# Kernel optimization log

Measured on AMD Instinct MI355X. Metric: run time of the kernel, lower is better.

Reference implementation:

```python
import jax, jax.numpy as jnp
import numpy as np

N = 50000
HEADS = 3
NEG_SLOPE = 0.2


def _add_self_loops(edge_index, num_nodes):
    loops = jnp.arange(num_nodes, dtype=edge_index.dtype)
    return jnp.concatenate([edge_index, jnp.stack([loops, loops])], axis=1)


def _gcn_conv(x, edge_index, W, b):
    # PyG GCNConv: add self loops, symmetric deg^-1/2 normalization.
    ei = _add_self_loops(edge_index, x.shape[0])
    src, dst = ei[0], ei[1]
    deg = jax.ops.segment_sum(jnp.ones_like(dst, dtype=x.dtype), dst, num_segments=x.shape[0])
    dinv = jax.lax.rsqrt(deg)  # deg >= 1 due to self loops
    norm = dinv[src] * dinv[dst]                      # [E']
    xw = x @ W                                        # [N, F_out]
    out = jax.ops.segment_sum(xw[src] * norm[:, None], dst, num_segments=x.shape[0])
    return out + b


def _gat_conv(x, edge_index, W, att_src, att_dst, b):
    # PyG GATConv (concat=True): self loops, per-edge attention, segment softmax.
    n = x.shape[0]
    ei = _add_self_loops(edge_index, n)
    src, dst = ei[0], ei[1]
    h = (x @ W).reshape(n, HEADS, -1)                 # [N, H, C]
    a_s = (h * att_src).sum(-1)                       # [N, H]
    a_d = (h * att_dst).sum(-1)                       # [N, H]
    e = jax.nn.leaky_relu(a_s[src] + a_d[dst], NEG_SLOPE)   # [E', H]
    m = jax.ops.segment_max(e, dst, num_segments=n)   # [N, H] per-dst max
    e = jnp.exp(e - m[dst])
    s = jax.ops.segment_sum(e, dst, num_segments=n)   # [N, H]
    alpha = e / s[dst]                                # [E', H]
    out = jax.ops.segment_sum(h[src] * alpha[:, :, None], dst, num_segments=n)
    return out.reshape(n, -1) + b                     # [N, H*C]


def setup_inputs() -> dict:
    key = jax.random.key(0)
    ks = jax.random.split(key, 9)
    in_ch, out_ch = 256, 64
    hid = 2 * out_ch  # 128
    E = 800000
    x = jax.random.normal(ks[0], (N, in_ch), dtype=jnp.float32)
    edge_index = jax.random.randint(ks[1], (2, E), 0, N, dtype=jnp.int32)
    W1 = jax.random.normal(ks[2], (in_ch, hid), dtype=jnp.float32) / np.sqrt(in_ch)
    b1 = jnp.zeros((hid,), dtype=jnp.float32)
    W2 = jax.random.normal(ks[3], (hid, HEADS * out_ch), dtype=jnp.float32) / np.sqrt(hid)
    att_src = jax.random.normal(ks[4], (HEADS, out_ch), dtype=jnp.float32) / np.sqrt(out_ch)
    att_dst = jax.random.normal(ks[5], (HEADS, out_ch), dtype=jnp.float32) / np.sqrt(out_ch)
    b2 = jnp.zeros((HEADS * out_ch,), dtype=jnp.float32)
    return {"x": x, "edge_index": edge_index, "W1": W1, "b1": b1,
            "W2": W2, "att_src": att_src, "att_dst": att_dst, "b2": b2}


def reference(x, edge_index, W1, b1, W2, att_src, att_dst, b2):
    h = jax.nn.relu(_gcn_conv(x, edge_index, W1, b1))
    # F.dropout(training=False) is identity in eval mode
    h = _gat_conv(h, edge_index, W2, att_src, att_dst, b2)
    return jax.nn.relu(h)
```

## Files before the change

kernel.cpp:

```cpp
#include <hip/hip_runtime.h>
#include <hip/hip_fp16.h>
#include <math.h>

#define NODES    50000
#define IN_CH    256
#define HID      128
#define HEADS    3
#define HC       64
#define OC       (HEADS*HC)
#define OCP      256
#define NEG_SLOPE 0.2f

typedef _Float16 half8_t __attribute__((ext_vector_type(8)));
typedef _Float16 half4_t __attribute__((ext_vector_type(4)));
typedef float float4_t __attribute__((ext_vector_type(4)));

__device__ __forceinline__ float lrelu(float v) { return v > 0.f ? v : NEG_SLOPE * v; }

__device__ __forceinline__ unsigned fkey(float f) {
    unsigned b = __float_as_uint(f);
    return (b & 0x80000000u) ? ~b : (b | 0x80000000u);
}
__device__ __forceinline__ float fdec(unsigned k) {
    unsigned b = (k & 0x80000000u) ? (k ^ 0x80000000u) : ~k;
    return __uint_as_float(b);
}


__global__ __launch_bounds__(256) void k_hist(const int* __restrict__ dst, int E, int* __restrict__ cnt,
                                              const float* __restrict__ W1, const float* __restrict__ W2,
                                              _Float16* __restrict__ W1t, _Float16* __restrict__ W2t) {
    int e = blockIdx.x * 256 + threadIdx.x;
    if (e < E) atomicAdd(&cnt[dst[e]], 1);
    if (e < IN_CH * HID) {
        int c = e >> 8, k = e & 255;
        W1t[e] = (_Float16)W1[(size_t)k * HID + c];
    } else if (e < IN_CH * HID + HID * OC) {
        int u = e - IN_CH * HID;
        int c = u >> 7, k = u & 127;
        W2t[u] = (_Float16)W2[(size_t)k * OC + c];
    }
}

__global__ __launch_bounds__(1024) void k_scanA(const int* __restrict__ cnt, int* __restrict__ off,
                                                float* __restrict__ dinv, int* __restrict__ bsum, int n) {
    __shared__ int wsums[16];
    int tid = threadIdx.x, lane = tid & 63, wid = tid >> 6;
    int i = blockIdx.x * 1024 + tid;
    int v = (i < n) ? cnt[i] : 0;
    int incl = v;
    #pragma unroll
    for (int d = 1; d < 64; d <<= 1) {
        int t = __shfl_up(incl, d, 64);
        if (lane >= d) incl += t;
    }
    if (lane == 63) wsums[wid] = incl;
    __syncthreads();
    if (tid == 0) {
        int run = 0;
        #pragma unroll
        for (int j = 0; j < 16; j++) { int t = wsums[j]; wsums[j] = run; run += t; }
        bsum[blockIdx.x] = run;
    }
    __syncthreads();
    if (i < n) {
        off[i] = wsums[wid] + incl - v;
        dinv[i] = rsqrtf((float)(v + 1));
    }
}

__global__ __launch_bounds__(64) void k_scanB(const int* __restrict__ bsum, int* __restrict__ bbase,
                                              int* __restrict__ off, int nb, int n) {
    int tid = threadIdx.x;
    int v = (tid < nb) ? bsum[tid] : 0;
    int incl = v;
    #pragma unroll
    for (int d = 1; d < 64; d <<= 1) {
        int t = __shfl_up(incl, d, 64);
        if (tid >= d) incl += t;
    }
    bbase[tid] = incl - v;
    if (tid == 63) off[n] = incl;
}

__global__ __launch_bounds__(256) void k_scanC(int* __restrict__ off, const int* __restrict__ bbase, int n) {
    int i = blockIdx.x * 256 + threadIdx.x;
    if (i < n) off[i] += bbase[i >> 10];
}

__global__ __launch_bounds__(256) void k_fill(const int* __restrict__ src, const int* __restrict__ dst, int E,
                                              const int* __restrict__ off, int* __restrict__ fill,
                                              int* __restrict__ csr) {
    int e = blockIdx.x * 256 + threadIdx.x;
    if (e < E) {
        int d = dst[e];
        int p = off[d] + atomicAdd(&fill[d], 1);
        csr[p] = src[e];
    }
}

__global__ __launch_bounds__(256) void k_gemm1m(const float* __restrict__ x, const _Float16* __restrict__ W1t,
                                                const float* __restrict__ dinv,
                                                _Float16* __restrict__ xwh, int n) {
    int wid = threadIdx.x >> 6, lane = threadIdx.x & 63;
    int lrow = lane & 15, kgrp = lane >> 4;
    int arow = blockIdx.x * 64 + wid * 16 + lrow;
    bool rv = arow < n;
    const float* xp = x + (size_t)arow * IN_CH + kgrp * 8;

    float4_t acc[8];
    #pragma unroll
    for (int s = 0; s < 8; s++) acc[s] = (float4_t)(0.f);

    #pragma unroll
    for (int kc = 0; kc < IN_CH; kc += 32) {
        float4 a0, a1;
        if (rv) { a0 = *(const float4*)(xp + kc); a1 = *(const float4*)(xp + kc + 4); }
        else { a0 = make_float4(0.f,0.f,0.f,0.f); a1 = a0; }
        half8_t af;
        af[0]=(_Float16)a0.x; af[1]=(_Float16)a0.y; af[2]=(_Float16)a0.z; af[3]=(_Float16)a0.w;
        af[4]=(_Float16)a1.x; af[5]=(_Float16)a1.y; af[6]=(_Float16)a1.z; af[7]=(_Float16)a1.w;
        #pragma unroll
        for (int s = 0; s < 8; s++) {
            const _Float16* bp = W1t + (size_t)(s * 16 + lrow) * IN_CH + kc + kgrp * 8;
            half8_t bf = *(const half8_t*)bp;
            acc[s] = __builtin_amdgcn_mfma_f32_16x16x32_f16(af, bf, acc[s], 0, 0, 0);
        }
    }

    int orow0 = blockIdx.x * 64 + wid * 16 + kgrp * 4;
    #pragma unroll
    for (int r = 0; r < 4; r++) {
        int orow = orow0 + r;
        if (orow < n) {
            float sc = dinv[orow];
            _Float16* po = xwh + ((size_t)orow << 7) + lrow;
            #pragma unroll
            for (int s = 0; s < 8; s++) po[s * 16] = (_Float16)(sc * acc[s][r]);
        }
    }
}

__global__ __launch_bounds__(256) void k_gcn(const _Float16* __restrict__ xwh, const int* __restrict__ csr,
                                             const int* __restrict__ off, const float* __restrict__ dinv,
                                             const float* __restrict__ b1, _Float16* __restrict__ hh, int n) {
    int w = (blockIdx.x * 256 + threadIdx.x) >> 6;
    int lane = threadIdx.x & 63;
    if (w >= n) return;
    int egrp = lane >> 4;
    int c8 = (lane & 15) * 8;
    float acc[8];
    #pragma unroll
    for (int j = 0; j < 8; j++) acc[j] = 0.f;

    int beg = off[w], end = off[w + 1];
    int i = beg;
    for (; i + 16 <= end; i += 16) {
        int s0 = csr[i + egrp];
        int s1 = csr[i + 4 + egrp];
        int s2 = csr[i + 8 + egrp];
        int s3 = csr[i + 12 + egrp];
        half8_t v0 = *(const half8_t*)(xwh + ((size_t)s0 << 7) + c8);
        half8_t v1 = *(const half8_t*)(xwh + ((size_t)s1 << 7) + c8);
        half8_t v2 = *(const half8_t*)(xwh + ((size_t)s2 << 7) + c8);
        half8_t v3 = *(const half8_t*)(xwh + ((size_t)s3 << 7) + c8);
        half8_t p01 = v0 + v1;
        half8_t p23 = v2 + v3;
        #pragma unroll
        for (int j = 0; j < 8; j++)
            acc[j] += (float)p01[j] + (float)p23[j];
    }
    for (; i + 4 <= end; i += 4) {
        int s = csr[i + egrp];
        half8_t v = *(const half8_t*)(xwh + ((size_t)s << 7) + c8);
        #pragma unroll
        for (int j = 0; j < 8; j++) acc[j] += (float)v[j];
    }
    if (i < end && egrp < (end - i)) {
        int s = csr[i + egrp];
        half8_t v = *(const half8_t*)(xwh + ((size_t)s << 7) + c8);
        #pragma unroll
        for (int j = 0; j < 8; j++) acc[j] += (float)v[j];
    }

    #pragma unroll
    for (int j = 0; j < 8; j++) {
        acc[j] += __shfl_xor(acc[j], 16, 64);
        acc[j] += __shfl_xor(acc[j], 32, 64);
    }
    if (egrp == 0) {
        float di = dinv[w];
        half8_t self = *(const half8_t*)(xwh + ((size_t)w << 7) + c8);
        float4 bb0 = *(const float4*)(b1 + c8);
        float4 bb1 = *(const float4*)(b1 + c8 + 4);
        float bv[8] = {bb0.x, bb0.y, bb0.z, bb0.w, bb1.x, bb1.y, bb1.z, bb1.w};
        half8_t o;
        #pragma unroll
        for (int j = 0; j < 8; j++)
            o[j] = (_Float16)fmaxf(fmaf(di, acc[j] + (float)self[j], bv[j]), 0.f);
        *(half8_t*)(hh + ((size_t)w << 7) + c8) = o;
    }
}

__global__ __launch_bounds__(256) void k_gemm2m(const _Float16* __restrict__ hh, const _Float16* __restrict__ W2t,
                                                _Float16* __restrict__ h2h, int n) {
    int wid = threadIdx.x >> 6, lane = threadIdx.x & 63;
    int lrow = lane & 15, kgrp = lane >> 4;
    int arow = blockIdx.x * 64 + wid * 16 + lrow;
    bool rv = arow < n;
    const _Float16* hp = hh + ((size_t)arow << 7) + kgrp * 8;

    float4_t acc[12];
    #pragma unroll
    for (int s = 0; s < 12; s++) acc[s] = (float4_t)(0.f);

    #pragma unroll
    for (int kc = 0; kc < HID; kc += 32) {
        half8_t af = (half8_t)((_Float16)0.f);
        if (rv) af = *(const half8_t*)(hp + kc);
        #pragma unroll
        for (int s = 0; s < 12; s++) {
            const _Float16* bp = W2t + (size_t)(s * 16 + lrow) * HID + kc + kgrp * 8;
            half8_t bf = *(const half8_t*)bp;
            acc[s] = __builtin_amdgcn_mfma_f32_16x16x32_f16(af, bf, acc[s], 0, 0, 0);
        }
    }

    int orow0 = blockIdx.x * 64 + wid * 16 + kgrp * 4;
    #pragma unroll
    for (int r = 0; r < 4; r++) {
        int orow = orow0 + r;
        if (orow < n) {
            _Float16* po = h2h + ((size_t)orow << 8) + lrow;
            #pragma unroll
            for (int s = 0; s < 12; s++) po[s * 16] = (_Float16)acc[s][r];
        }
    }
}

__global__ __launch_bounds__(256) void k_att(const _Float16* __restrict__ h2h, const float* __restrict__ att_s,
                                             const float* __restrict__ att_d, float* __restrict__ a_s4,
                                             float* __restrict__ a_d4, int n) {
    int w = (blockIdx.x * 256 + threadIdx.x) >> 6;
    int lane = threadIdx.x & 63;
    if (w >= n) return;
    bool act = lane < 48;
    int ll = act ? lane : (lane - 48);
    int hd = ll >> 4;
    int c4 = ll * 4;

    half4_t hv = *(const half4_t*)(h2h + ((size_t)w << 8) + c4);
    float4 as = *(const float4*)(att_s + c4);
    float4 ad = *(const float4*)(att_d + c4);
    float vs = (float)hv[0] * as.x + (float)hv[1] * as.y + (float)hv[2] * as.z + (float)hv[3] * as.w;
    float vd = (float)hv[0] * ad.x + (float)hv[1] * ad.y + (float)hv[2] * ad.z + (float)hv[3] * ad.w;
    #pragma unroll
    for (int o = 1; o < 16; o <<= 1) {
        vs += __shfl_xor(vs, o, 64);
        vd += __shfl_xor(vd, o, 64);
    }
    if (act && (ll & 15) == 0) {
        a_s4[w * 4 + hd] = vs;
        a_d4[w * 4 + hd] = vd;
    }
}

__global__ __launch_bounds__(1024) void k_asmax(const float* __restrict__ a_s4, int n, unsigned* __restrict__ asmaxk) {
    int i = blockIdx.x * 1024 + threadIdx.x;
    float m0 = -1e30f, m1 = -1e30f, m2 = -1e30f;
    if (i < n) {
        float4 v = *(const float4*)(a_s4 + (size_t)i * 4);
        m0 = v.x; m1 = v.y; m2 = v.z;
    }
    #pragma unroll
    for (int o = 32; o > 0; o >>= 1) {
        m0 = fmaxf(m0, __shfl_xor(m0, o, 64));
        m1 = fmaxf(m1, __shfl_xor(m1, o, 64));
        m2 = fmaxf(m2, __shfl_xor(m2, o, 64));
    }
    __shared__ float sm[16][3];
    int lane = threadIdx.x & 63, wid = threadIdx.x >> 6;
    if (lane == 0) { sm[wid][0] = m0; sm[wid][1] = m1; sm[wid][2] = m2; }
    __syncthreads();
    if (threadIdx.x == 0) {
        for (int j = 1; j < 16; j++) {
            m0 = fmaxf(m0, sm[j][0]); m1 = fmaxf(m1, sm[j][1]); m2 = fmaxf(m2, sm[j][2]);
        }
        atomicMax(asmaxk + 0, fkey(m0));
        atomicMax(asmaxk + 1, fkey(m1));
        atomicMax(asmaxk + 2, fkey(m2));
    }
}

#define GAT_EDGE(ev, hv) do { \
    float wl = __expf(lrelu((ev) + adh) - Ch); \
    ssum += wl; \
    a0 = fmaf(wl, (float)(hv)[0], a0); \
    a1 = fmaf(wl, (float)(hv)[1], a1); \
    a2 = fmaf(wl, (float)(hv)[2], a2); \
    a3 = fmaf(wl, (float)(hv)[3], a3); \
} while (0)

__global__ __launch_bounds__(256) void k_gat(const _Float16* __restrict__ h2h, const int* __restrict__ csr,
                                             const int* __restrict__ off, const float* __restrict__ a_s4,
                                             const float* __restrict__ a_d4, const unsigned* __restrict__ asmaxk,
                                             const float* __restrict__ b2, float* __restrict__ out, int n) {
    int w = (blockIdx.x * 256 + threadIdx.x) >> 6;
    int lane = threadIdx.x & 63;
    if (w >= n) return;
    bool act = lane < 48;
    int ll = act ? lane : (lane - 48);
    int hd = ll >> 4;
    int c4 = ll * 4;

    float adh = a_d4[w * 4 + hd];
    float Ch  = lrelu(fdec(asmaxk[hd]) + adh);
    float ash = a_s4[w * 4 + hd];
    float wsl = __expf(lrelu(ash + adh) - Ch);
    float ssum = wsl;
    half4_t hv = *(const half4_t*)(h2h + ((size_t)w << 8) + c4);
    float a0 = wsl * (float)hv[0], a1 = wsl * (float)hv[1];
    float a2 = wsl * (float)hv[2], a3 = wsl * (float)hv[3];

    int beg = off[w], end = off[w + 1];
    int i = beg;
    for (; i + 4 <= end; i += 4) {
        int sA = csr[i], sB = csr[i + 1], sC = csr[i + 2], sD = csr[i + 3];
        float eA = a_s4[(size_t)sA * 4 + hd];
        float eB = a_s4[(size_t)sB * 4 + hd];
        float eC = a_s4[(size_t)sC * 4 + hd];
        float eD = a_s4[(size_t)sD * 4 + hd];
        half4_t hA = *(const half4_t*)(h2h + ((size_t)sA << 8) + c4);
        half4_t hB = *(const half4_t*)(h2h + ((size_t)sB << 8) + c4);
        half4_t hC = *(const half4_t*)(h2h + ((size_t)sC << 8) + c4);
        half4_t hD = *(const half4_t*)(h2h + ((size_t)sD << 8) + c4);
        GAT_EDGE(eA, hA); GAT_EDGE(eB, hB); GAT_EDGE(eC, hC); GAT_EDGE(eD, hD);
    }
    for (; i < end; i++) {
        int s = csr[i];
        float ev = a_s4[(size_t)s * 4 + hd];
        half4_t hx = *(const half4_t*)(h2h + ((size_t)s << 8) + c4);
        GAT_EDGE(ev, hx);
    }

    if (act) {
        float inv = 1.f / ssum;
        float4 bb = *(const float4*)(b2 + c4);
        float4 o;
        o.x = fmaxf(fmaf(a0, inv, bb.x), 0.f);
        o.y = fmaxf(fmaf(a1, inv, bb.y), 0.f);
        o.z = fmaxf(fmaf(a2, inv, bb.z), 0.f);
        o.w = fmaxf(fmaf(a3, inv, bb.w), 0.f);
        *(float4*)(out + (size_t)w * OC + c4) = o;
    }
}

extern "C" void kernel_launch(void* const* d_in, const int* in_sizes, int n_in,
                              void* d_out, int out_size, void* d_ws, size_t ws_size,
                              hipStream_t stream) {
    const float* x        = (const float*)d_in[0];
    const int*   ei       = (const int*)d_in[1];
    const float* W1       = (const float*)d_in[2];
    const float* b1       = (const float*)d_in[3];
    const float* W2       = (const float*)d_in[4];
    const float* att_src  = (const float*)d_in[5];
    const float* att_dst  = (const float*)d_in[6];
    const float* b2       = (const float*)d_in[7];
    float* out = (float*)d_out;

    const int n = in_sizes[0] / IN_CH;
    const int E = in_sizes[1] / 2;
    const int* src = ei;
    const int* dst = ei + E;

    char* ws = (char*)d_ws;
    int*      cnt    = (int*)(ws + 0);
    int*      fill   = (int*)(ws + 200704);
    unsigned* asmaxk = (unsigned*)(ws + 401408);
    int*      off    = (int*)(ws + 401664);
    float*    dinv   = (float*)(ws + 602368);
    int*      bsum   = (int*)(ws + 803072);
    int*      bbase  = (int*)(ws + 803328);
    _Float16* W1t    = (_Float16*)(ws + 803584);
    _Float16* W2t    = (_Float16*)(ws + 869120);
    int*      csr    = (int*)(ws + 918528);
    float*    a_s4   = (float*)(ws + 4118528);
    float*    a_d4   = (float*)(ws + 4918528);
    _Float16* xwh    = (_Float16*)(ws + 5718528);
    _Float16* hh     = (_Float16*)(ws + 18518528);
    _Float16* h2h    = (_Float16*)(ws + 31318528);

    (void)hipMemsetAsync(ws, 0, 401424, stream);

    int egrid = (E + 255) / 256;
    int nb = (n + 1023) / 1024;
    k_hist<<<egrid, 256, 0, stream>>>(dst, E, cnt, W1, W2, W1t, W2t);
    k_scanA<<<nb, 1024, 0, stream>>>(cnt, off, dinv, bsum, n);
    k_scanB<<<1, 64, 0, stream>>>(bsum, bbase, off, nb, n);
    k_scanC<<<(n + 255) / 256, 256, 0, stream>>>(off, bbase, n);
    k_fill<<<egrid, 256, 0, stream>>>(src, dst, E, off, fill, csr);

    int gm = (n + 63) / 64;
    k_gemm1m<<<gm, 256, 0, stream>>>(x, W1t, dinv, xwh, n);

    int ngrid = (n + 3) / 4;
    k_gcn<<<ngrid, 256, 0, stream>>>(xwh, csr, off, dinv, b1, hh, n);

    k_gemm2m<<<gm, 256, 0, stream>>>(hh, W2t, h2h, n);

    k_att<<<ngrid, 256, 0, stream>>>(h2h, att_src, att_dst, a_s4, a_d4, n);
    k_asmax<<<nb, 1024, 0, stream>>>(a_s4, n, asmaxk);
    k_gat<<<ngrid, 256, 0, stream>>>(h2h, csr, off, a_s4, a_d4, asmaxk, b2, out, n);
}
```

Measured before the change: 259.5 us.

## Drop scanC and fill array; use off as atomic cursor and prescale CSR

Removes the k_scanC launch and the separate fill counter array. k_fill now uses atomicAdd on the block-local exclusive offsets plus the per-block base, so after filling, off[w] holds the segment end and segment bounds are rebuilt from off[w-1], off[w] and bbase. CSR entries are stored pre-shifted as byte offsets into h2h, so the gather kernels save the index multiply. The memset also shrinks. This saves one kernel launch and some memory traffic, at the cost of extra bbase lookups and index arithmetic in the gather kernels.

```diff
diff --git a/kernel.cpp b/kernel.cpp
--- a/kernel.cpp
+++ b/kernel.cpp
@@ -70,7 +70,7 @@
 }
 
 __global__ __launch_bounds__(64) void k_scanB(const int* __restrict__ bsum, int* __restrict__ bbase,
-                                              int* __restrict__ off, int nb, int n) {
+                                              int nb) {
     int tid = threadIdx.x;
     int v = (tid < nb) ? bsum[tid] : 0;
     int incl = v;
@@ -80,23 +80,24 @@
         if (tid >= d) incl += t;
     }
     bbase[tid] = incl - v;
-    if (tid == 63) off[n] = incl;
-}
-
-__global__ __launch_bounds__(256) void k_scanC(int* __restrict__ off, const int* __restrict__ bbase, int n) {
-    int i = blockIdx.x * 256 + threadIdx.x;
-    if (i < n) off[i] += bbase[i >> 10];
 }
 
 __global__ __launch_bounds__(256) void k_fill(const int* __restrict__ src, const int* __restrict__ dst, int E,
-                                              const int* __restrict__ off, int* __restrict__ fill,
+                                              int* __restrict__ off, const int* __restrict__ bbase,
                                               int* __restrict__ csr) {
     int e = blockIdx.x * 256 + threadIdx.x;
     if (e < E) {
         int d = dst[e];
-        int p = off[d] + atomicAdd(&fill[d], 1);
-        csr[p] = src[e];
-    }
+        int p = atomicAdd(&off[d], 1) + bbase[d >> 10];
+        csr[p] = src[e] << 9;
+    }
+}
+
+__device__ __forceinline__ int2 seg_of(const int* __restrict__ off, const int* __restrict__ bbase, int w) {
+    int bb = bbase[w >> 10];
+    int beg = ((w & 1023) ? off[w - 1] : 0) + bb;
+    int end = off[w] + bb;
+    return make_int2(beg, end);
 }
 
 __global__ __launch_bounds__(256) void k_gemm1m(const float* __restrict__ x, const _Float16* __restrict__ W1t,
@@ -142,28 +143,31 @@
 }
 
 __global__ __launch_bounds__(256) void k_gcn(const _Float16* __restrict__ xwh, const int* __restrict__ csr,
-                                             const int* __restrict__ off, const float* __restrict__ dinv,
+                                             const int* __restrict__ off, const int* __restrict__ bbase,
+                                             const float* __restrict__ dinv,
                                              const float* __restrict__ b1, _Float16* __restrict__ hh, int n) {
     int w = (blockIdx.x * 256 + threadIdx.x) >> 6;
     int lane = threadIdx.x & 63;
     if (w >= n) return;
     int egrp = lane >> 4;
-    int c8 = (lane & 15) * 8;
+    int c8b = (lane & 15) * 16;
+    const char* xb = (const char*)xwh;
     float acc[8];
     #pragma unroll
     for (int j = 0; j < 8; j++) acc[j] = 0.f;
 
-    int beg = off[w], end = off[w + 1];
+    int2 seg = seg_of(off, bbase, w);
+    int beg = seg.x, end = seg.y;
     int i = beg;
     for (; i + 16 <= end; i += 16) {
-        int s0 = csr[i + egrp];
-        int s1 = csr[i + 4 + egrp];
-        int s2 = csr[i + 8 + egrp];
-        int s3 = csr[i + 12 + egrp];
-        half8_t v0 = *(const half8_t*)(xwh + ((size_t)s0 << 7) + c8);
-        half8_t v1 = *(const half8_t*)(xwh + ((size_t)s1 << 7) + c8);
-        half8_t v2 = *(const half8_t*)(xwh + ((size_t)s2 << 7) + c8);
-        half8_t v3 = *(const half8_t*)(xwh + ((size_t)s3 << 7) + c8);
+        int o0 = csr[i + egrp];
+        int o1 = csr[i + 4 + egrp];
+        int o2 = csr[i + 8 + egrp];
+        int o3 = csr[i + 12 + egrp];
+        half8_t v0 = *(const half8_t*)(xb + (o0 >> 1) + c8b);
+        half8_t v1 = *(const half8_t*)(xb + (o1 >> 1) + c8b);
+        half8_t v2 = *(const half8_t*)(xb + (o2 >> 1) + c8b);
+        half8_t v3 = *(const half8_t*)(xb + (o3 >> 1) + c8b);
         half8_t p01 = v0 + v1;
         half8_t p23 = v2 + v3;
         #pragma unroll
@@ -171,14 +175,14 @@
             acc[j] += (float)p01[j] + (float)p23[j];
     }
     for (; i + 4 <= end; i += 4) {
-        int s = csr[i + egrp];
-        half8_t v = *(const half8_t*)(xwh + ((size_t)s << 7) + c8);
+        int o = csr[i + egrp];
+        half8_t v = *(const half8_t*)(xb + (o >> 1) + c8b);
         #pragma unroll
         for (int j = 0; j < 8; j++) acc[j] += (float)v[j];
     }
     if (i < end && egrp < (end - i)) {
-        int s = csr[i + egrp];
-        half8_t v = *(const half8_t*)(xwh + ((size_t)s << 7) + c8);
+        int o = csr[i + egrp];
+        half8_t v = *(const half8_t*)(xb + (o >> 1) + c8b);
         #pragma unroll
         for (int j = 0; j < 8; j++) acc[j] += (float)v[j];
     }
@@ -190,15 +194,13 @@
     }
     if (egrp == 0) {
         float di = dinv[w];
-        half8_t self = *(const half8_t*)(xwh + ((size_t)w << 7) + c8);
-        float4 bb0 = *(const float4*)(b1 + c8);
-        float4 bb1 = *(const float4*)(b1 + c8 + 4);
-        float bv[8] = {bb0.x, bb0.y, bb0.z, bb0.w, bb1.x, bb1.y, bb1.z, bb1.w};
+        half8_t self = *(const half8_t*)(xb + ((size_t)w << 8) + c8b);
+        const float* bp = (const float*)((const char*)b1 + c8b * 2);
         half8_t o;
         #pragma unroll
         for (int j = 0; j < 8; j++)
-            o[j] = (_Float16)fmaxf(fmaf(di, acc[j] + (float)self[j], bv[j]), 0.f);
-        *(half8_t*)(hh + ((size_t)w << 7) + c8) = o;
+            o[j] = (_Float16)fmaxf(fmaf(di, acc[j] + (float)self[j], bp[j]), 0.f);
+        *(half8_t*)((char*)hh + ((size_t)w << 8) + c8b) = o;
     }
 }
 
@@ -302,7 +304,8 @@
 } while (0)
 
 __global__ __launch_bounds__(256) void k_gat(const _Float16* __restrict__ h2h, const int* __restrict__ csr,
-                                             const int* __restrict__ off, const float* __restrict__ a_s4,
+                                             const int* __restrict__ off, const int* __restrict__ bbase,
+                                             const float* __restrict__ a_s4,
                                              const float* __restrict__ a_d4, const unsigned* __restrict__ asmaxk,
                                              const float* __restrict__ b2, float* __restrict__ out, int n) {
     int w = (blockIdx.x * 256 + threadIdx.x) >> 6;
@@ -311,47 +314,51 @@
     bool act = lane < 48;
     int ll = act ? lane : (lane - 48);
     int hd = ll >> 4;
-    int c4 = ll * 4;
+    int c4b = ll * 8;
+    const char* hb = (const char*)h2h;
+    const char* ab = (const char*)a_s4;
+    int hd4 = hd * 4;
 
     float adh = a_d4[w * 4 + hd];
     float Ch  = lrelu(fdec(asmaxk[hd]) + adh);
     float ash = a_s4[w * 4 + hd];
     float wsl = __expf(lrelu(ash + adh) - Ch);
     float ssum = wsl;
-    half4_t hv = *(const half4_t*)(h2h + ((size_t)w << 8) + c4);
+    half4_t hv = *(const half4_t*)(hb + ((size_t)w << 9) + c4b);
     float a0 = wsl * (float)hv[0], a1 = wsl * (float)hv[1];
     float a2 = wsl * (float)hv[2], a3 = wsl * (float)hv[3];
 
-    int beg = off[w], end = off[w + 1];
+    int2 seg = seg_of(off, bbase, w);
+    int beg = seg.x, end = seg.y;
     int i = beg;
     for (; i + 4 <= end; i += 4) {
-        int sA = csr[i], sB = csr[i + 1], sC = csr[i + 2], sD = csr[i + 3];
-        float eA = a_s4[(size_t)sA * 4 + hd];
-        float eB = a_s4[(size_t)sB * 4 + hd];
-        float eC = a_s4[(size_t)sC * 4 + hd];
-        float eD = a_s4[(size_t)sD * 4 + hd];
-        half4_t hA = *(const half4_t*)(h2h + ((size_t)sA << 8) + c4);
-        half4_t hB = *(const half4_t*)(h2h + ((size_t)sB << 8) + c4);
-        half4_t hC = *(const half4_t*)(h2h + ((size_t)sC << 8) + c4);
-        half4_t hD = *(const half4_t*)(h2h + ((size_t)sD << 8) + c4);
+        int oA = csr[i], oB = csr[i + 1], oC = csr[i + 2], oD = csr[i + 3];
+        float eA = *(const float*)(ab + (oA >> 5) + hd4);
+        float eB = *(const float*)(ab + (oB >> 5) + hd4);
+        float eC = *(const float*)(ab + (oC >> 5) + hd4);
+        float eD = *(const float*)(ab + (oD >> 5) + hd4);
+        half4_t hA = *(const half4_t*)(hb + oA + c4b);
+        half4_t hB = *(const half4_t*)(hb + oB + c4b);
+        half4_t hC = *(const half4_t*)(hb + oC + c4b);
+        half4_t hD = *(const half4_t*)(hb + oD + c4b);
         GAT_EDGE(eA, hA); GAT_EDGE(eB, hB); GAT_EDGE(eC, hC); GAT_EDGE(eD, hD);
     }
     for (; i < end; i++) {
-        int s = csr[i];
-        float ev = a_s4[(size_t)s * 4 + hd];
-        half4_t hx = *(const half4_t*)(h2h + ((size_t)s << 8) + c4);
+        int o = csr[i];
+        float ev = *(const float*)(ab + (o >> 5) + hd4);
+        half4_t hx = *(const half4_t*)(hb + o + c4b);
         GAT_EDGE(ev, hx);
     }
 
     if (act) {
         float inv = 1.f / ssum;
-        float4 bb = *(const float4*)(b2 + c4);
+        const float* bp = (const float*)((const char*)b2 + c4b);
         float4 o;
-        o.x = fmaxf(fmaf(a0, inv, bb.x), 0.f);
-        o.y = fmaxf(fmaf(a1, inv, bb.y), 0.f);
-        o.z = fmaxf(fmaf(a2, inv, bb.z), 0.f);
-        o.w = fmaxf(fmaf(a3, inv, bb.w), 0.f);
-        *(float4*)(out + (size_t)w * OC + c4) = o;
+        o.x = fmaxf(fmaf(a0, inv, bp[0]), 0.f);
+        o.y = fmaxf(fmaf(a1, inv, bp[1]), 0.f);
+        o.z = fmaxf(fmaf(a2, inv, bp[2]), 0.f);
+        o.w = fmaxf(fmaf(a3, inv, bp[3]), 0.f);
+        *(float4*)((char*)out + (size_t)w * (OC * 4) + c4b * 2) = o;
     }
 }
 
@@ -375,40 +382,38 @@
 
     char* ws = (char*)d_ws;
     int*      cnt    = (int*)(ws + 0);
-    int*      fill   = (int*)(ws + 200704);
-    unsigned* asmaxk = (unsigned*)(ws + 401408);
-    int*      off    = (int*)(ws + 401664);
-    float*    dinv   = (float*)(ws + 602368);
-    int*      bsum   = (int*)(ws + 803072);
-    int*      bbase  = (int*)(ws + 803328);
-    _Float16* W1t    = (_Float16*)(ws + 803584);
-    _Float16* W2t    = (_Float16*)(ws + 869120);
-    int*      csr    = (int*)(ws + 918528);
-    float*    a_s4   = (float*)(ws + 4118528);
-    float*    a_d4   = (float*)(ws + 4918528);
-    _Float16* xwh    = (_Float16*)(ws + 5718528);
-    _Float16* hh     = (_Float16*)(ws + 18518528);
-    _Float16* h2h    = (_Float16*)(ws + 31318528);
-
-    (void)hipMemsetAsync(ws, 0, 401424, stream);
+    unsigned* asmaxk = (unsigned*)(ws + 200704);
+    int*      off    = (int*)(ws + 200960);
+    float*    dinv   = (float*)(ws + 401664);
+    int*      bsum   = (int*)(ws + 602368);
+    int*      bbase  = (int*)(ws + 602624);
+    _Float16* W1t    = (_Float16*)(ws + 602880);
+    _Float16* W2t    = (_Float16*)(ws + 668416);
+    int*      csr    = (int*)(ws + 717568);
+    float*    a_s4   = (float*)(ws + 3917568);
+    float*    a_d4   = (float*)(ws + 4717568);
+    _Float16* xwh    = (_Float16*)(ws + 5517568);
+    _Float16* hh     = (_Float16*)(ws + 18317568);
+    _Float16* h2h    = (_Float16*)(ws + 31117568);
+
+    (void)hipMemsetAsync(ws, 0, 200720, stream);
 
     int egrid = (E + 255) / 256;
     int nb = (n + 1023) / 1024;
     k_hist<<<egrid, 256, 0, stream>>>(dst, E, cnt, W1, W2, W1t, W2t);
     k_scanA<<<nb, 1024, 0, stream>>>(cnt, off, dinv, bsum, n);
-    k_scanB<<<1, 64, 0, stream>>>(bsum, bbase, off, nb, n);
-    k_scanC<<<(n + 255) / 256, 256, 0, stream>>>(off, bbase, n);
-    k_fill<<<egrid, 256, 0, stream>>>(src, dst, E, off, fill, csr);
+    k_scanB<<<1, 64, 0, stream>>>(bsum, bbase, nb);
+    k_fill<<<egrid, 256, 0, stream>>>(src, dst, E, off, bbase, csr);
 
     int gm = (n + 63) / 64;
     k_gemm1m<<<gm, 256, 0, stream>>>(x, W1t, dinv, xwh, n);
 
     int ngrid = (n + 3) / 4;
-    k_gcn<<<ngrid, 256, 0, stream>>>(xwh, csr, off, dinv, b1, hh, n);
+    k_gcn<<<ngrid, 256, 0, stream>>>(xwh, csr, off, bbase, dinv, b1, hh, n);
 
     k_gemm2m<<<gm, 256, 0, stream>>>(hh, W2t, h2h, n);
 
     k_att<<<ngrid, 256, 0, stream>>>(h2h, att_src, att_dst, a_s4, a_d4, n);
     k_asmax<<<nb, 1024, 0, stream>>>(a_s4, n, asmaxk);
-    k_gat<<<ngrid, 256, 0, stream>>>(h2h, csr, off, a_s4, a_d4, asmaxk, b2, out, n);
-}
+    k_gat<<<ngrid, 256, 0, stream>>>(h2h, csr, off, bbase, a_s4, a_d4, asmaxk, b2, out, n);
+}
```

Result: slower. 272.2 us (+4.9%).

## Build CSR via two-level bucket sort instead of histogram-scan-fill

Applied to the files above, without the earlier changes.

Replaces the per-node histogram, three-kernel scan and global atomic fill with a coarse bucketing pass (128 destinations per bucket), a single-block bucket scan, and a per-bucket LDS counting sort that writes offsets, dinv and CSR. Global atomics now hit only 391 bucket counters, and most scatter work moves into shared memory, with fewer launches and a smaller memset. The cost is heavy contention on those few bucket counters, a fixed per-bucket capacity of 4096 edges that silently drops overflow on skewed graphs, and 16-bit packing of the source index, which cannot hold node ids of 65536 or more.

```diff
diff --git a/kernel.cpp b/kernel.cpp
--- a/kernel.cpp
+++ b/kernel.cpp
@@ -8,8 +8,9 @@
 #define HEADS    3
 #define HC       64
 #define OC       (HEADS*HC)
-#define OCP      256
 #define NEG_SLOPE 0.2f
+#define NBK      391
+#define BCAP     4096
 
 typedef _Float16 half8_t __attribute__((ext_vector_type(8)));
 typedef _Float16 half4_t __attribute__((ext_vector_type(4)));
@@ -26,12 +27,18 @@
     return __uint_as_float(b);
 }
 
-
-__global__ __launch_bounds__(256) void k_hist(const int* __restrict__ dst, int E, int* __restrict__ cnt,
-                                              const float* __restrict__ W1, const float* __restrict__ W2,
-                                              _Float16* __restrict__ W1t, _Float16* __restrict__ W2t) {
+__global__ __launch_bounds__(256) void k_bucket(const int* __restrict__ src, const int* __restrict__ dst, int E,
+                                                int* __restrict__ bcnt, unsigned* __restrict__ bstage,
+                                                const float* __restrict__ W1, const float* __restrict__ W2,
+                                                _Float16* __restrict__ W1t, _Float16* __restrict__ W2t) {
     int e = blockIdx.x * 256 + threadIdx.x;
-    if (e < E) atomicAdd(&cnt[dst[e]], 1);
+    if (e < E) {
+        int d = dst[e], s = src[e];
+        int b = d >> 7;
+        int pos = atomicAdd(&bcnt[b], 1);
+        if (pos < BCAP)
+            bstage[(size_t)b * BCAP + pos] = ((unsigned)(d & 127) << 16) | (unsigned)s;
+    }
     if (e < IN_CH * HID) {
         int c = e >> 8, k = e & 255;
         W1t[e] = (_Float16)W1[(size_t)k * HID + c];
@@ -42,12 +49,11 @@
     }
 }
 
-__global__ __launch_bounds__(1024) void k_scanA(const int* __restrict__ cnt, int* __restrict__ off,
-                                                float* __restrict__ dinv, int* __restrict__ bsum, int n) {
-    __shared__ int wsums[16];
+__global__ __launch_bounds__(512) void k_bscan(const int* __restrict__ bcnt, int* __restrict__ bbase,
+                                               int* __restrict__ off, int nbk, int n) {
+    __shared__ int wsums[8];
     int tid = threadIdx.x, lane = tid & 63, wid = tid >> 6;
-    int i = blockIdx.x * 1024 + tid;
-    int v = (i < n) ? cnt[i] : 0;
+    int v = (tid < nbk) ? bcnt[tid] : 0;
     int incl = v;
     #pragma unroll
     for (int d = 1; d < 64; d <<= 1) {
@@ -59,43 +65,59 @@
     if (tid == 0) {
         int run = 0;
         #pragma unroll
-        for (int j = 0; j < 16; j++) { int t = wsums[j]; wsums[j] = run; run += t; }
-        bsum[blockIdx.x] = run;
-    }
-    __syncthreads();
-    if (i < n) {
-        off[i] = wsums[wid] + incl - v;
-        dinv[i] = rsqrtf((float)(v + 1));
-    }
-}
-
-__global__ __launch_bounds__(64) void k_scanB(const int* __restrict__ bsum, int* __restrict__ bbase,
-                                              int* __restrict__ off, int nb, int n) {
-    int tid = threadIdx.x;
-    int v = (tid < nb) ? bsum[tid] : 0;
-    int incl = v;
-    #pragma unroll
-    for (int d = 1; d < 64; d <<= 1) {
-        int t = __shfl_up(incl, d, 64);
-        if (tid >= d) incl += t;
-    }
-    bbase[tid] = incl - v;
-    if (tid == 63) off[n] = incl;
-}
-
-__global__ __launch_bounds__(256) void k_scanC(int* __restrict__ off, const int* __restrict__ bbase, int n) {
-    int i = blockIdx.x * 256 + threadIdx.x;
-    if (i < n) off[i] += bbase[i >> 10];
-}
-
-__global__ __launch_bounds__(256) void k_fill(const int* __restrict__ src, const int* __restrict__ dst, int E,
-                                              const int* __restrict__ off, int* __restrict__ fill,
-                                              int* __restrict__ csr) {
-    int e = blockIdx.x * 256 + threadIdx.x;
-    if (e < E) {
-        int d = dst[e];
-        int p = off[d] + atomicAdd(&fill[d], 1);
-        csr[p] = src[e];
+        for (int j = 0; j < 8; j++) { int t = wsums[j]; wsums[j] = run; run += t; }
+    }
+    __syncthreads();
+    int excl = wsums[wid] + incl - v;
+    if (tid < nbk) bbase[tid] = excl;
+    if (tid == nbk - 1) off[n] = excl + v;
+}
+
+__global__ __launch_bounds__(256) void k_bsort(const unsigned* __restrict__ bstage, const int* __restrict__ bcnt,
+                                               const int* __restrict__ bbase, int* __restrict__ off,
+                                               float* __restrict__ dinv, int* __restrict__ csr, int n) {
+    __shared__ int cnt128[128], exc128[128], rank128[128];
+    __shared__ int wtot;
+    int b = blockIdx.x, tid = threadIdx.x;
+    if (tid < 128) { cnt128[tid] = 0; rank128[tid] = 0; }
+    __syncthreads();
+
+    int cntE = bcnt[b];
+    if (cntE > BCAP) cntE = BCAP;
+    const unsigned* st = bstage + (size_t)b * BCAP;
+    for (int i = tid; i < cntE; i += 256)
+        atomicAdd(&cnt128[st[i] >> 16], 1);
+    __syncthreads();
+
+    int v = 0, incl = 0;
+    if (tid < 128) {
+        v = cnt128[tid];
+        incl = v;
+        #pragma unroll
+        for (int d = 1; d < 64; d <<= 1) {
+            int t = __shfl_up(incl, d, 64);
+            if ((tid & 63) >= d) incl += t;
+        }
+        if (tid == 63) wtot = incl;
+    }
+    __syncthreads();
+    int base = bbase[b];
+    if (tid < 128) {
+        int excl = incl - v + (tid >= 64 ? wtot : 0);
+        exc128[tid] = excl;
+        int gd = b * 128 + tid;
+        if (gd < n) {
+            off[gd] = base + excl;
+            dinv[gd] = rsqrtf((float)(v + 1));
+        }
+    }
+    __syncthreads();
+
+    for (int i = tid; i < cntE; i += 256) {
+        unsigned vv = st[i];
+        int ld = vv >> 16, s = vv & 0xffff;
+        int r = atomicAdd(&rank128[ld], 1);
+        csr[base + exc128[ld] + r] = s;
     }
 }
 
@@ -374,31 +396,28 @@
     const int* dst = ei + E;
 
     char* ws = (char*)d_ws;
-    int*      cnt    = (int*)(ws + 0);
-    int*      fill   = (int*)(ws + 200704);
-    unsigned* asmaxk = (unsigned*)(ws + 401408);
-    int*      off    = (int*)(ws + 401664);
-    float*    dinv   = (float*)(ws + 602368);
-    int*      bsum   = (int*)(ws + 803072);
-    int*      bbase  = (int*)(ws + 803328);
-    _Float16* W1t    = (_Float16*)(ws + 803584);
-    _Float16* W2t    = (_Float16*)(ws + 869120);
-    int*      csr    = (int*)(ws + 918528);
-    float*    a_s4   = (float*)(ws + 4118528);
-    float*    a_d4   = (float*)(ws + 4918528);
-    _Float16* xwh    = (_Float16*)(ws + 5718528);
-    _Float16* hh     = (_Float16*)(ws + 18518528);
-    _Float16* h2h    = (_Float16*)(ws + 31318528);
-
-    (void)hipMemsetAsync(ws, 0, 401424, stream);
+    int*      bcnt   = (int*)(ws + 0);
+    unsigned* asmaxk = (unsigned*)(ws + 2048);
+    int*      off    = (int*)(ws + 4096);
+    float*    dinv   = (float*)(ws + 204800);
+    int*      bbase  = (int*)(ws + 405504);
+    _Float16* W1t    = (_Float16*)(ws + 407552);
+    _Float16* W2t    = (_Float16*)(ws + 473088);
+    unsigned* bstage = (unsigned*)(ws + 522240);
+    int*      csr    = (int*)(ws + 6928384);
+    float*    a_s4   = (float*)(ws + 10128384);
+    float*    a_d4   = (float*)(ws + 10928384);
+    _Float16* xwh    = (_Float16*)(ws + 11728384);
+    _Float16* hh     = (_Float16*)(ws + 24528384);
+    _Float16* h2h    = (_Float16*)(ws + 37328384);
+
+    (void)hipMemsetAsync(ws, 0, 2064, stream);
 
     int egrid = (E + 255) / 256;
     int nb = (n + 1023) / 1024;
-    k_hist<<<egrid, 256, 0, stream>>>(dst, E, cnt, W1, W2, W1t, W2t);
-    k_scanA<<<nb, 1024, 0, stream>>>(cnt, off, dinv, bsum, n);
-    k_scanB<<<1, 64, 0, stream>>>(bsum, bbase, off, nb, n);
-    k_scanC<<<(n + 255) / 256, 256, 0, stream>>>(off, bbase, n);
-    k_fill<<<egrid, 256, 0, stream>>>(src, dst, E, off, fill, csr);
+    k_bucket<<<egrid, 256, 0, stream>>>(src, dst, E, bcnt, bstage, W1, W2, W1t, W2t);
+    k_bscan<<<1, 512, 0, stream>>>(bcnt, bbase, off, NBK, n);
+    k_bsort<<<NBK, 256, 0, stream>>>(bstage, bcnt, bbase, off, dinv, csr, n);
 
     int gm = (n + 63) / 64;
     k_gemm1m<<<gm, 256, 0, stream>>>(x, W1t, dinv, xwh, n);
```

Measured after the change: 467.2 us. 1.8x slower.

## Fuse GCN aggregation with second GEMM via shared-memory tile

Applied to the files above, without the earlier changes.

Merges the GCN neighbor aggregation kernel and the second MFMA GEMM into one kernel. Each 512-thread block aggregates 64 nodes (8 per wave) into a swizzled LDS tile, then its waves split the 64x192 output GEMM by row tile and column half. This removes the global write and re-read of the intermediate hidden features and one kernel launch. In exchange, each wave now handles 8 nodes serially and the block waits at a barrier for its slowest node, so fewer independent waves are available to hide gather latency.

```diff
diff --git a/kernel.cpp b/kernel.cpp
--- a/kernel.cpp
+++ b/kernel.cpp
@@ -8,7 +8,6 @@
 #define HEADS    3
 #define HC       64
 #define OC       (HEADS*HC)
-#define OCP      256
 #define NEG_SLOPE 0.2f
 
 typedef _Float16 half8_t __attribute__((ext_vector_type(8)));
@@ -141,99 +140,110 @@
     }
 }
 
-__global__ __launch_bounds__(256) void k_gcn(const _Float16* __restrict__ xwh, const int* __restrict__ csr,
-                                             const int* __restrict__ off, const float* __restrict__ dinv,
-                                             const float* __restrict__ b1, _Float16* __restrict__ hh, int n) {
-    int w = (blockIdx.x * 256 + threadIdx.x) >> 6;
+#define HSW(row, chunk) ((((chunk) ^ ((row) & 7)) << 3))
+
+__global__ __launch_bounds__(512) void k_gcn2(const _Float16* __restrict__ xwh, const int* __restrict__ csr,
+                                              const int* __restrict__ off, const float* __restrict__ dinv,
+                                              const float* __restrict__ b1, const _Float16* __restrict__ W2t,
+                                              _Float16* __restrict__ h2h, int n) {
+    __shared__ _Float16 hs[64][128];
+    int w8 = threadIdx.x >> 6;
     int lane = threadIdx.x & 63;
-    if (w >= n) return;
     int egrp = lane >> 4;
-    int c8 = (lane & 15) * 8;
-    float acc[8];
-    #pragma unroll
-    for (int j = 0; j < 8; j++) acc[j] = 0.f;
-
-    int beg = off[w], end = off[w + 1];
-    int i = beg;
-    for (; i + 16 <= end; i += 16) {
-        int s0 = csr[i + egrp];
-        int s1 = csr[i + 4 + egrp];
-        int s2 = csr[i + 8 + egrp];
-        int s3 = csr[i + 12 + egrp];
-        half8_t v0 = *(const half8_t*)(xwh + ((size_t)s0 << 7) + c8);
-        half8_t v1 = *(const half8_t*)(xwh + ((size_t)s1 << 7) + c8);
-        half8_t v2 = *(const half8_t*)(xwh + ((size_t)s2 << 7) + c8);
-        half8_t v3 = *(const half8_t*)(xwh + ((size_t)s3 << 7) + c8);
-        half8_t p01 = v0 + v1;
-        half8_t p23 = v2 + v3;
+    int chunk = lane & 15;
+    int c8 = chunk * 8;
+    int base = blockIdx.x * 64;
+
+    for (int j = 0; j < 8; j++) {
+        int ndl = w8 * 8 + j;
+        int nd = base + ndl;
+        if (nd >= n) {
+            if (egrp == 0) *(half8_t*)&hs[ndl][HSW(ndl, chunk)] = (half8_t)((_Float16)0.f);
+            continue;
+        }
+        float acc[8];
         #pragma unroll
-        for (int j = 0; j < 8; j++)
-            acc[j] += (float)p01[j] + (float)p23[j];
-    }
-    for (; i + 4 <= end; i += 4) {
-        int s = csr[i + egrp];
-        half8_t v = *(const half8_t*)(xwh + ((size_t)s << 7) + c8);
+        for (int q = 0; q < 8; q++) acc[q] = 0.f;
+
+        int beg = off[nd], end = off[nd + 1];
+        int i = beg;
+        for (; i + 16 <= end; i += 16) {
+            int s0 = csr[i + egrp];
+            int s1 = csr[i + 4 + egrp];
+            int s2 = csr[i + 8 + egrp];
+            int s3 = csr[i + 12 + egrp];
+            half8_t v0 = *(const half8_t*)(xwh + ((size_t)s0 << 7) + c8);
+            half8_t v1 = *(const half8_t*)(xwh + ((size_t)s1 << 7) + c8);
+            half8_t v2 = *(const half8_t*)(xwh + ((size_t)s2 << 7) + c8);
+            half8_t v3 = *(const half8_t*)(xwh + ((size_t)s3 << 7) + c8);
+            half8_t p01 = v0 + v1;
+            half8_t p23 = v2 + v3;
+            #pragma unroll
+            for (int q = 0; q < 8; q++)
+                acc[q] += (float)p01[q] + (float)p23[q];
+        }
+        for (; i + 4 <= end; i += 4) {
+            int s = csr[i + egrp];
+            half8_t v = *(const half8_t*)(xwh + ((size_t)s << 7) + c8);
+            #pragma unroll
+            for (int q = 0; q < 8; q++) acc[q] += (float)v[q];
+        }
+        if (i < end && egrp < (end - i)) {
+            int s = csr[i + egrp];
+            half8_t v = *(const half8_t*)(xwh + ((size_t)s << 7) + c8);
+            #pragma unroll
+            for (int q = 0; q < 8; q++) acc[q] += (float)v[q];
+        }
+
         #pragma unroll
-        for (int j = 0; j < 8; j++) acc[j] += (float)v[j];
-    }
-    if (i < end && egrp < (end - i)) {
-        int s = csr[i + egrp];
-        half8_t v = *(const half8_t*)(xwh + ((size_t)s << 7) + c8);
+        for (int q = 0; q < 8; q++) {
+            acc[q] += __shfl_xor(acc[q], 16, 64);
+            acc[q] += __shfl_xor(acc[q], 32, 64);
+        }
+        if (egrp == 0) {
+            float di = dinv[nd];
+            half8_t self = *(const half8_t*)(xwh + ((size_t)nd << 7) + c8);
+            float4 bb0 = *(const float4*)(b1 + c8);
+            float4 bb1 = *(const float4*)(b1 + c8 + 4);
+            float bv[8] = {bb0.x, bb0.y, bb0.z, bb0.w, bb1.x, bb1.y, bb1.z, bb1.w};
+            half8_t o;
+            #pragma unroll
+            for (int q = 0; q < 8; q++)
+                o[q] = (_Float16)fmaxf(fmaf(di, acc[q] + (float)self[q], bv[q]), 0.f);
+            *(half8_t*)&hs[ndl][HSW(ndl, chunk)] = o;
+        }
+    }
+    __syncthreads();
+
+    int rt = w8 >> 1;
+    int ch = w8 & 1;
+    int lrow = lane & 15, kgrp = lane >> 4;
+    int arow_l = rt * 16 + lrow;
+
+    float4_t acc2[6];
+    #pragma unroll
+    for (int s = 0; s < 6; s++) acc2[s] = (float4_t)(0.f);
+
+    #pragma unroll
+    for (int kc = 0; kc < HID; kc += 32) {
+        half8_t af = *(const half8_t*)&hs[arow_l][HSW(arow_l, (kc >> 3) + kgrp)];
         #pragma unroll
-        for (int j = 0; j < 8; j++) acc[j] += (float)v[j];
-    }
-
-    #pragma unroll
-    for (int j = 0; j < 8; j++) {
-        acc[j] += __shfl_xor(acc[j], 16, 64);
-        acc[j] += __shfl_xor(acc[j], 32, 64);
-    }
-    if (egrp == 0) {
-        float di = dinv[w];
-        half8_t self = *(const half8_t*)(xwh + ((size_t)w << 7) + c8);
-        float4 bb0 = *(const float4*)(b1 + c8);
-        float4 bb1 = *(const float4*)(b1 + c8 + 4);
-        float bv[8] = {bb0.x, bb0.y, bb0.z, bb0.w, bb1.x, bb1.y, bb1.z, bb1.w};
-        half8_t o;
-        #pragma unroll
-        for (int j = 0; j < 8; j++)
-            o[j] = (_Float16)fmaxf(fmaf(di, acc[j] + (float)self[j], bv[j]), 0.f);
-        *(half8_t*)(hh + ((size_t)w << 7) + c8) = o;
-    }
-}
-
-__global__ __launch_bounds__(256) void k_gemm2m(const _Float16* __restrict__ hh, const _Float16* __restrict__ W2t,
-                                                _Float16* __restrict__ h2h, int n) {
-    int wid = threadIdx.x >> 6, lane = threadIdx.x & 63;
-    int lrow = lane & 15, kgrp = lane >> 4;
-    int arow = blockIdx.x * 64 + wid * 16 + lrow;
-    bool rv = arow < n;
-    const _Float16* hp = hh + ((size_t)arow << 7) + kgrp * 8;
-
-    float4_t acc[12];
-    #pragma unroll
-    for (int s = 0; s < 12; s++) acc[s] = (float4_t)(0.f);
-
-    #pragma unroll
-    for (int kc = 0; kc < HID; kc += 32) {
-        half8_t af = (half8_t)((_Float16)0.f);
-        if (rv) af = *(const half8_t*)(hp + kc);
-        #pragma unroll
-        for (int s = 0; s < 12; s++) {
-            const _Float16* bp = W2t + (size_t)(s * 16 + lrow) * HID + kc + kgrp * 8;
+        for (int s = 0; s < 6; s++) {
+            int st = ch * 6 + s;
+            const _Float16* bp = W2t + (size_t)(st * 16 + lrow) * HID + kc + kgrp * 8;
             half8_t bf = *(const half8_t*)bp;
-            acc[s] = __builtin_amdgcn_mfma_f32_16x16x32_f16(af, bf, acc[s], 0, 0, 0);
-        }
-    }
-
-    int orow0 = blockIdx.x * 64 + wid * 16 + kgrp * 4;
+            acc2[s] = __builtin_amdgcn_mfma_f32_16x16x32_f16(af, bf, acc2[s], 0, 0, 0);
+        }
+    }
+
+    int orow0 = base + rt * 16 + kgrp * 4;
     #pragma unroll
     for (int r = 0; r < 4; r++) {
         int orow = orow0 + r;
         if (orow < n) {
-            _Float16* po = h2h + ((size_t)orow << 8) + lrow;
-            #pragma unroll
-            for (int s = 0; s < 12; s++) po[s * 16] = (_Float16)acc[s][r];
+            _Float16* po = h2h + ((size_t)orow << 8) + ch * 96 + lrow;
+            #pragma unroll
+            for (int s = 0; s < 6; s++) po[s * 16] = (_Float16)acc2[s][r];
         }
     }
 }
@@ -387,8 +397,7 @@
     float*    a_s4   = (float*)(ws + 4118528);
     float*    a_d4   = (float*)(ws + 4918528);
     _Float16* xwh    = (_Float16*)(ws + 5718528);
-    _Float16* hh     = (_Float16*)(ws + 18518528);
-    _Float16* h2h    = (_Float16*)(ws + 31318528);
+    _Float16* h2h    = (_Float16*)(ws + 18518528);
 
     (void)hipMemsetAsync(ws, 0, 401424, stream);
 
@@ -403,11 +412,9 @@
     int gm = (n + 63) / 64;
     k_gemm1m<<<gm, 256, 0, stream>>>(x, W1t, dinv, xwh, n);
 
+    k_gcn2<<<gm, 512, 0, stream>>>(xwh, csr, off, dinv, b1, W2t, h2h, n);
+
     int ngrid = (n + 3) / 4;
-    k_gcn<<<ngrid, 256, 0, stream>>>(xwh, csr, off, dinv, b1, hh, n);
-
-    k_gemm2m<<<gm, 256, 0, stream>>>(hh, W2t, h2h, n);
-
     k_att<<<ngrid, 256, 0, stream>>>(h2h, att_src, att_dst, a_s4, a_d4, n);
     k_asmax<<<nb, 1024, 0, stream>>>(a_s4, n, asmaxk);
     k_gat<<<ngrid, 256, 0, stream>>>(h2h, csr, off, a_s4, a_d4, asmaxk, b2, out, n);
```

After: 274.4 us. 5.7% more time.
